# Kernel tuning notes

Hardware: AMD Instinct MI355X
Metric: run time of the kernel (lower is better)

## Reference

```python
import jax, jax.numpy as jnp
import numpy as np

EPS = 1e-5

def _bn(x, gamma, beta, axes):
    # batch-norm with batch statistics (torch training-mode forward, biased var)
    mu = jnp.mean(x, axis=axes, keepdims=True)
    var = jnp.var(x, axis=axes, keepdims=True)
    shape = [1] * x.ndim
    shape[1] = -1  # channel dim is axis 1
    return (x - mu) * jax.lax.rsqrt(var + EPS) * gamma.reshape(shape) + beta.reshape(shape)

def setup_inputs() -> dict:
    key = jax.random.key(0)
    k1, k2, k3, k4, k5 = jax.random.split(key, 5)
    N, H, D, L, M, C = 8, 8, 64, 1024, 1024, 64
    scale = 1.0 / np.sqrt(D)
    return {
        "query": jax.random.normal(k1, (N, H, D, L), dtype=jnp.float32) * scale,
        "key": jax.random.normal(k2, (N, H, D, M), dtype=jnp.float32) * scale,
        "value": jax.random.normal(k3, (N, H, C, M), dtype=jnp.float32),
        "gamma_sim": jnp.ones((H,), dtype=jnp.float32),
        "beta_sim": jnp.zeros((H,), dtype=jnp.float32),
        "gamma_v": jnp.ones((H * C,), dtype=jnp.float32),
        "beta_v": jnp.zeros((H * C,), dtype=jnp.float32),
    }

def reference(query, key, value, gamma_sim, beta_sim, gamma_v, beta_v):
    N, H, D, L = query.shape
    C = value.shape[2]
    # QK^T -> [N, H, L, M]
    logits = jnp.einsum('bhdl,bhdm->bhlm', query, key)
    # BatchNorm2d over channel=head: stats over (N, L, M)
    logits = _bn(logits, gamma_sim, beta_sim, axes=(0, 2, 3))
    # softmax in fp32 (autocast(enabled=False) + .float())
    weights = jax.nn.softmax(logits.astype(jnp.float32), axis=-1)
    # AV -> [N, H, D_v, L] then flatten heads
    rv = jnp.einsum('bhlm,bhdm->bhdl', weights, value).reshape(N, H * C, L)
    # BatchNorm1d over channel: stats over (N, L)
    rv = _bn(rv, gamma_v, beta_v, axes=(0, 2))
    # torch F.gelu default is exact (erf-based)
    return jax.nn.gelu(rv, approximate=False)
```

## Files before the change

kernel.cpp:

```cpp
#include <hip/hip_runtime.h>
#include <hip/hip_bf16.h>
#include <math.h>


typedef __attribute__((ext_vector_type(4)))  float    f32x4;
typedef __attribute__((ext_vector_type(16))) float    f32x16;
typedef __attribute__((ext_vector_type(8)))  __bf16   bf16x8;
typedef __attribute__((ext_vector_type(8)))  short    s16x8;
typedef __attribute__((ext_vector_type(4)))  short    s16x4;
typedef __attribute__((ext_vector_type(2)))  unsigned u32x2;
typedef __attribute__((ext_vector_type(4)))  unsigned u32x4;

#define KT_OFF 0u
#define VB_OFF (8u*1024u*1024u)
#define P1_OFF (16u*1024u*1024u)
#define RS_OFF (24u*1024u*1024u)
#define GM_OFF (32u*1024u*1024u)
#define SPLIT_WS_NEED (24u*1024u*1024u + 512u*1024u + 4096u)
#define GRAM2_WS_NEED (48u*1024u*1024u)

static __device__ __forceinline__ short bf16s(float f) {
  return __builtin_bit_cast(short, (__bf16)f);
}
static __device__ __forceinline__ unsigned pkbf(float lo, float hi) {
  unsigned l = (unsigned)__builtin_bit_cast(unsigned short, (__bf16)lo);
  unsigned h = (unsigned)__builtin_bit_cast(unsigned short, (__bf16)hi);
  return l | (h << 16);
}
static __device__ __forceinline__ float bf2f(short s) {
  return __builtin_bit_cast(float, ((unsigned)(unsigned short)s) << 16);
}
static __device__ __forceinline__ bf16x8 cvt8(const float* p) {
  f32x4 a = *(const f32x4*)p;
  f32x4 b = *(const f32x4*)(p + 4);
  bf16x8 r;
  r[0]=(__bf16)a[0]; r[1]=(__bf16)a[1]; r[2]=(__bf16)a[2]; r[3]=(__bf16)a[3];
  r[4]=(__bf16)b[0]; r[5]=(__bf16)b[1]; r[6]=(__bf16)b[2]; r[7]=(__bf16)b[3];
  return r;
}
static __device__ __forceinline__ f32x16 z16() {
  f32x16 z;
  #pragma unroll
  for (int i = 0; i < 16; ++i) z[i] = 0.f;
  return z;
}
static __device__ __forceinline__ bf16x8 mk8(unsigned a, unsigned b, unsigned c, unsigned d) {
  u32x4 u; u[0]=a; u[1]=b; u[2]=c; u[3]=d;
  return __builtin_bit_cast(bf16x8, u);
}
static __device__ __forceinline__ void gll16(const void* g, void* l) {
  __builtin_amdgcn_global_load_lds(
      (const __attribute__((address_space(1))) void*)g,
      (__attribute__((address_space(3))) void*)l, 16, 0, 0);
}

__global__ __launch_bounds__(256) void k0_prep(const float* __restrict__ K,
                                               const float* __restrict__ V,
                                               short* __restrict__ Kt,
                                               short* __restrict__ Vb) {
  int tid = threadIdx.x;
  if (blockIdx.x < 1024) {
    int bh = blockIdx.x >> 4;
    int m0 = (blockIdx.x & 15) << 6;
    __shared__ short tile[64][72];
    int d = tid >> 2;
    #pragma unroll
    for (int it = 0; it < 4; ++it) {
      int mc4 = (tid & 3) + (it << 2);
      const f32x4 v = *(const f32x4*)(K + (((size_t)(bh*64 + d)) << 10) + m0 + (mc4 << 2));
      #pragma unroll
      for (int j = 0; j < 4; ++j) tile[mc4*4 + j][d] = bf16s(v[j]);
    }
    __syncthreads();
    int m = tid >> 2, q = tid & 3;
    s16x8 o0, o1;
    #pragma unroll
    for (int j = 0; j < 8; ++j) { o0[j] = tile[m][q*16 + j]; o1[j] = tile[m][q*16 + 8 + j]; }
    short* dst = Kt + ((size_t)bh << 16) + ((size_t)(m0 + m) << 6) + (q << 4);
    *(s16x8*)dst = o0;
    *(s16x8*)(dst + 8) = o1;
  } else {
    size_t base = ((size_t)(blockIdx.x - 1024)) << 13;
    #pragma unroll
    for (int it = 0; it < 8; ++it) {
      size_t idx = base + ((size_t)it << 10) + (tid << 2);
      f32x4 x = *(const f32x4*)(V + idx);
      s16x4 y;
      #pragma unroll
      for (int j = 0; j < 4; ++j) y[j] = bf16s(x[j]);
      *(s16x4*)(Vb + idx) = y;
    }
  }
}

__global__ __launch_bounds__(256) void k1a_gram(const float* __restrict__ Q,
                                                const float* __restrict__ K,
                                                float* __restrict__ gm) {
  int bh = blockIdx.x >> 3, sl = blockIdx.x & 7;
  int tid = threadIdx.x, w = tid >> 6, lane = tid & 63;
  int l31 = lane & 31, hi = lane >> 5;
  const float* qlo = Q + ((size_t)bh << 16) + ((size_t)l31 << 10);
  const float* qhi = qlo + (32u << 10);
  const float* klo = K + ((size_t)bh << 16) + ((size_t)l31 << 10);
  const float* khi = klo + (32u << 10);
  f32x16 gq00 = z16(), gq01 = z16(), gq11 = z16();
  f32x16 gk00 = z16(), gk01 = z16(), gk11 = z16();
  #pragma unroll
  for (int lc = 0; lc < 2; ++lc) {
    int loff = (sl << 7) + (w << 5) + (lc << 4) + (hi << 3);
    bf16x8 aql = cvt8(qlo + loff), aqh = cvt8(qhi + loff);
    bf16x8 akl = cvt8(klo + loff), akh = cvt8(khi + loff);
    gq00 = __builtin_amdgcn_mfma_f32_32x32x16_bf16(aql, aql, gq00, 0, 0, 0);
    gq01 = __builtin_amdgcn_mfma_f32_32x32x16_bf16(aql, aqh, gq01, 0, 0, 0);
    gq11 = __builtin_amdgcn_mfma_f32_32x32x16_bf16(aqh, aqh, gq11, 0, 0, 0);
    gk00 = __builtin_amdgcn_mfma_f32_32x32x16_bf16(akl, akl, gk00, 0, 0, 0);
    gk01 = __builtin_amdgcn_mfma_f32_32x32x16_bf16(akl, akh, gk01, 0, 0, 0);
    gk11 = __builtin_amdgcn_mfma_f32_32x32x16_bf16(akh, akh, gk11, 0, 0, 0);
  }
  __shared__ float RQ[4][64][16];
  __shared__ float RK[4][64][16];
  float* gout = gm + ((size_t)blockIdx.x * 6144u);
  #define K1A_RED(GQ_, GK_, TI_)                                            \
    __syncthreads();                                                        \
    _Pragma("unroll")                                                       \
    for (int r = 0; r < 16; ++r) { RQ[w][lane][r] = GQ_[r]; RK[w][lane][r] = GK_[r]; } \
    __syncthreads();                                                        \
    {                                                                       \
      int e = tid & 63, rq = (tid >> 6) << 2;                               \
      f32x4 aq, ak;                                                         \
      _Pragma("unroll")                                                     \
      for (int j = 0; j < 4; ++j) {                                         \
        int r = rq + j;                                                     \
        aq[j] = RQ[0][e][r] + RQ[1][e][r] + RQ[2][e][r] + RQ[3][e][r];      \
        ak[j] = RK[0][e][r] + RK[1][e][r] + RK[2][e][r] + RK[3][e][r];      \
      }                                                                     \
      *(f32x4*)(gout + (TI_)*1024 + (e << 4) + rq) = aq;                    \
      *(f32x4*)(gout + ((TI_) + 3)*1024 + (e << 4) + rq) = ak;              \
    }
  K1A_RED(gq00, gk00, 0)
  K1A_RED(gq01, gk01, 1)
  K1A_RED(gq11, gk11, 2)
  #undef K1A_RED
}

__global__ __launch_bounds__(256) void k1b_dot(const float* __restrict__ gm,
                                               float* __restrict__ ss) {
  int bh = blockIdx.x;
  int tid = threadIdx.x, w = tid >> 6, lane = tid & 63;
  float part = 0.f;
  #pragma unroll
  for (int t = 0; t < 3; ++t) {
    f32x4 aq = {0.f, 0.f, 0.f, 0.f}, ak = {0.f, 0.f, 0.f, 0.f};
    #pragma unroll
    for (int s = 0; s < 8; ++s) {
      const float* base = gm + ((size_t)((bh << 3) + s) * 6144u) + (size_t)t*1024u + (tid << 2);
      aq += *(const f32x4*)base;
      ak += *(const f32x4*)(base + 3*1024);
    }
    float d = aq[0]*ak[0] + aq[1]*ak[1] + aq[2]*ak[2] + aq[3]*ak[3];
    part += (t == 1) ? 2.0f * d : d;
  }
  #pragma unroll
  for (int off = 32; off > 0; off >>= 1) part += __shfl_down(part, off, 64);
  __shared__ float red[4];
  if (lane == 0) red[w] = part;
  __syncthreads();
  if (tid == 0) ss[bh] = red[0] + red[1] + red[2] + red[3];
}

__global__ __launch_bounds__(512) void k1_gram(const float* __restrict__ Q,
                                               const float* __restrict__ K,
                                               float* __restrict__ ss) {
  int bh = blockIdx.x;
  int tid = threadIdx.x, w = tid >> 6, lane = tid & 63;
  int l31 = lane & 31, hi = lane >> 5;
  const float* qlo = Q + ((size_t)bh << 16) + ((size_t)l31 << 10);
  const float* qhi = qlo + (32u << 10);
  const float* klo = K + ((size_t)bh << 16) + ((size_t)l31 << 10);
  const float* khi = klo + (32u << 10);
  f32x16 gq00 = z16(), gq01 = z16(), gq11 = z16();
  f32x16 gk00 = z16(), gk01 = z16(), gk11 = z16();
  for (int lc = 0; lc < 8; ++lc) {
    int loff = (w << 7) + (lc << 4) + (hi << 3);
    bf16x8 aql = cvt8(qlo + loff), aqh = cvt8(qhi + loff);
    bf16x8 akl = cvt8(klo + loff), akh = cvt8(khi + loff);
    gq00 = __builtin_amdgcn_mfma_f32_32x32x16_bf16(aql, aql, gq00, 0, 0, 0);
    gq01 = __builtin_amdgcn_mfma_f32_32x32x16_bf16(aql, aqh, gq01, 0, 0, 0);
    gq11 = __builtin_amdgcn_mfma_f32_32x32x16_bf16(aqh, aqh, gq11, 0, 0, 0);
    gk00 = __builtin_amdgcn_mfma_f32_32x32x16_bf16(akl, akl, gk00, 0, 0, 0);
    gk01 = __builtin_amdgcn_mfma_f32_32x32x16_bf16(akl, akh, gk01, 0, 0, 0);
    gk11 = __builtin_amdgcn_mfma_f32_32x32x16_bf16(akh, akh, gk11, 0, 0, 0);
  }
  __shared__ float RQ[8][64][16];
  __shared__ float RK[8][64][16];
  float part = 0.f;
  #define K1_REDUCE(GQ_, GK_, WT_)                                          \
    __syncthreads();                                                        \
    _Pragma("unroll")                                                       \
    for (int r = 0; r < 16; ++r) { RQ[w][lane][r] = GQ_[r]; RK[w][lane][r] = GK_[r]; } \
    __syncthreads();                                                        \
    if (tid < 256) {                                                        \
      int e = tid & 63, rq = (tid >> 6) << 2;                               \
      _Pragma("unroll")                                                     \
      for (int j = 0; j < 4; ++j) {                                         \
        int r = rq + j;                                                     \
        float aq = 0.f, ak = 0.f;                                           \
        _Pragma("unroll")                                                   \
        for (int ww = 0; ww < 8; ++ww) { aq += RQ[ww][e][r]; ak += RK[ww][e][r]; } \
        part += (WT_) * aq * ak;                                            \
      }                                                                     \
    }
  K1_REDUCE(gq00, gk00, 1.0f)
  K1_REDUCE(gq01, gk01, 2.0f)
  K1_REDUCE(gq11, gk11, 1.0f)
  #undef K1_REDUCE
  #pragma unroll
  for (int off = 32; off > 0; off >>= 1) part += __shfl_down(part, off, 64);
  __shared__ float red[8];
  __syncthreads();
  if (lane == 0) red[w] = part;
  __syncthreads();
  if (tid == 0) {
    float s = 0.f;
    #pragma unroll
    for (int ww = 0; ww < 8; ++ww) s += red[ww];
    ss[bh] = s;
  }
}

template<bool SPLIT>
__global__ __launch_bounds__(256) void k2_attn(const float* __restrict__ Q,
                                               const short* __restrict__ Kt,
                                               const short* __restrict__ Vbf,
                                               const float* __restrict__ ss,
                                               const float* __restrict__ gsim,
                                               float* __restrict__ rv,
                                               short* __restrict__ p1,
                                               float* __restrict__ rsp) {
  __shared__ short ldsK[2][4096];
  __shared__ short ldsV[2][4096];
  int b = blockIdx.x;
  int bh   = (b & 7) + (((b >> 3) & 7) << 3);
  int rest = b >> 6;
  int slab  = SPLIT ? (rest >> 1) : rest;
  int mh    = SPLIT ? (rest & 1) : 0;
  int tbase = mh << 3;
  const int TT = SPLIT ? 8 : 16;
  int l0 = slab << 7;
  int tid = threadIdx.x, w = tid >> 6, lane = tid & 63;
  int l31 = lane & 31, hi = lane >> 5;
  int lq = l0 + (w << 5) + l31;

  int h = bh & 7;
  float ssum = 0.f;
  #pragma unroll
  for (int nb = 0; nb < 8; ++nb) ssum += ss[(nb << 3) + h];
  float scf = gsim[h] * rsqrtf(ssum * (1.0f / 8388608.0f) + 1e-5f) * 1.44269504089f;

  const short* ktb = Kt  + ((size_t)bh << 16);
  const short* vbb = Vbf + ((size_t)bh << 16);
  const float* qb  = Q   + ((size_t)bh << 16) + lq;

  bf16x8 qf[4];
  #pragma unroll
  for (int kc = 0; kc < 4; ++kc) {
    bf16x8 f;
    #pragma unroll
    for (int i = 0; i < 8; ++i)
      f[i] = (__bf16)(qb[(size_t)((kc << 4) + (hi << 3) + i) << 10] * scf);
    qf[kc] = f;
  }

  int koff[2][4], voff[2][2][2];
  #pragma unroll
  for (int mt = 0; mt < 2; ++mt) {
    int mrow = (mt << 5) + l31;
    #pragma unroll
    for (int kc = 0; kc < 4; ++kc) {
      int chunk = (kc << 1) + hi;
      koff[mt][kc] = mrow*128 + ((chunk << 4) ^ ((mrow & 7) << 4));
    }
    #pragma unroll
    for (int cz = 0; cz < 2; ++cz) {
      int crow = (cz << 5) + l31;
      #pragma unroll
      for (int j = 0; j < 2; ++j) {
        int chunk = (mt << 2) + (j << 1) + hi;
        voff[mt][cz][j] = crow*128 + ((chunk << 4) ^ ((crow & 7) << 4));
      }
    }
  }

  {
    int m0 = tbase << 6;
    #pragma unroll
    for (int p = 0; p < 2; ++p) {
      int idx = (p << 8) + tid, row = idx >> 3, ch = idx & 7;
      gll16(ktb + ((size_t)(m0 + row) << 6) + ((ch ^ (row & 7)) << 3), &ldsK[0][idx << 3]);
      gll16(vbb + ((size_t)row << 10) + m0 + ((ch ^ (row & 7)) << 3), &ldsV[0][idx << 3]);
    }
  }
  __syncthreads();

  f32x16 o0 = z16(), o1 = z16();
  float rsum = 0.f;

  for (int t = 0; t < TT; ++t) {
    int cur = t & 1, nxt = cur ^ 1;
    if (t < TT - 1) {
      int m1 = (tbase + t + 1) << 6;
      #pragma unroll
      for (int p = 0; p < 2; ++p) {
        int idx = (p << 8) + tid, row = idx >> 3, ch = idx & 7;
        gll16(ktb + ((size_t)(m1 + row) << 6) + ((ch ^ (row & 7)) << 3), &ldsK[nxt][idx << 3]);
        gll16(vbb + ((size_t)row << 10) + m1 + ((ch ^ (row & 7)) << 3), &ldsV[nxt][idx << 3]);
      }
    }
    #pragma unroll
    for (int mt = 0; mt < 2; ++mt) {
      f32x16 s = z16();
      __builtin_amdgcn_s_setprio(1);
      #pragma unroll
      for (int kc = 0; kc < 4; ++kc) {
        bf16x8 af = *(bf16x8*)((char*)&ldsK[cur][0] + koff[mt][kc]);
        s = __builtin_amdgcn_mfma_f32_32x32x16_bf16(af, qf[kc], s, 0, 0, 0);
      }
      __builtin_amdgcn_s_setprio(0);
      float p[16];
      #pragma unroll
      for (int r = 0; r < 16; ++r) { p[r] = __builtin_amdgcn_exp2f(s[r]); rsum += p[r]; }
      unsigned dw[8];
      #pragma unroll
      for (int j = 0; j < 8; ++j) dw[j] = pkbf(p[2*j], p[2*j+1]);
      u32x2 a0 = __builtin_amdgcn_permlane32_swap(dw[0], dw[2], false, false);
      u32x2 a1 = __builtin_amdgcn_permlane32_swap(dw[1], dw[3], false, false);
      u32x2 a2 = __builtin_amdgcn_permlane32_swap(dw[4], dw[6], false, false);
      u32x2 a3 = __builtin_amdgcn_permlane32_swap(dw[5], dw[7], false, false);
      bf16x8 pb0 = mk8(a0[0], a1[0], a0[1], a1[1]);
      bf16x8 pb1 = mk8(a2[0], a3[0], a2[1], a3[1]);
      __builtin_amdgcn_s_setprio(1);
      {
        bf16x8 va0 = *(bf16x8*)((char*)&ldsV[cur][0] + voff[mt][0][0]);
        o0 = __builtin_amdgcn_mfma_f32_32x32x16_bf16(va0, pb0, o0, 0, 0, 0);
        bf16x8 va1 = *(bf16x8*)((char*)&ldsV[cur][0] + voff[mt][0][1]);
        o0 = __builtin_amdgcn_mfma_f32_32x32x16_bf16(va1, pb1, o0, 0, 0, 0);
      }
      {
        bf16x8 va0 = *(bf16x8*)((char*)&ldsV[cur][0] + voff[mt][1][0]);
        o1 = __builtin_amdgcn_mfma_f32_32x32x16_bf16(va0, pb0, o1, 0, 0, 0);
        bf16x8 va1 = *(bf16x8*)((char*)&ldsV[cur][0] + voff[mt][1][1]);
        o1 = __builtin_amdgcn_mfma_f32_32x32x16_bf16(va1, pb1, o1, 0, 0, 0);
      }
      __builtin_amdgcn_s_setprio(0);
    }
    __syncthreads();
  }

  float tot = rsum + __shfl_xor(rsum, 32, 64);
  if constexpr (!SPLIT) {
    float inv = 1.0f / tot;
    #pragma unroll
    for (int r = 0; r < 16; ++r) {
      int cr = (r & 3) + ((r >> 2) << 3) + (hi << 2);
      rv[((size_t)(bh*64 + cr) << 10) + lq] = o0[r] * inv;
    }
    #pragma unroll
    for (int r = 0; r < 16; ++r) {
      int cr = 32 + (r & 3) + ((r >> 2) << 3) + (hi << 2);
      rv[((size_t)(bh*64 + cr) << 10) + lq] = o1[r] * inv;
    }
  } else {
    if (mh == 0) {
      #pragma unroll
      for (int r = 0; r < 16; ++r) {
        int cr = (r & 3) + ((r >> 2) << 3) + (hi << 2);
        rv[((size_t)(bh*64 + cr) << 10) + lq] = o0[r];
      }
      #pragma unroll
      for (int r = 0; r < 16; ++r) {
        int cr = 32 + (r & 3) + ((r >> 2) << 3) + (hi << 2);
        rv[((size_t)(bh*64 + cr) << 10) + lq] = o1[r];
      }
    } else {
      #pragma unroll
      for (int r = 0; r < 16; ++r) {
        int cr = (r & 3) + ((r >> 2) << 3) + (hi << 2);
        p1[((size_t)(bh*64 + cr) << 10) + lq] = bf16s(o0[r]);
      }
      #pragma unroll
      for (int r = 0; r < 16; ++r) {
        int cr = 32 + (r & 3) + ((r >> 2) << 3) + (hi << 2);
        p1[((size_t)(bh*64 + cr) << 10) + lq] = bf16s(o1[r]);
      }
    }
    if (hi == 0) rsp[(mh << 16) + (bh << 10) + lq] = tot;
  }
}

template<bool SPLIT>
__global__ __launch_bounds__(256) void k34_bn_gelu(const float* rv,
                                                   const short* __restrict__ p1,
                                                   const float* __restrict__ rsp,
                                                   const float* __restrict__ gamma_v,
                                                   const float* __restrict__ beta_v,
                                                   float* out) {
  int ch = blockIdx.x;
  int h  = ch >> 6;
  int tid = threadIdx.x, w = tid >> 6, lane = tid & 63;
  f32x4 xr[8];
  float s = 0.f, s2 = 0.f;
  #pragma unroll
  for (int b = 0; b < 8; ++b) {
    size_t roff = (((size_t)(b*512 + ch)) << 10) + (tid << 2);
    f32x4 x = *(const f32x4*)(rv + roff);
    if constexpr (SPLIT) {
      s16x4 pp = *(const s16x4*)(p1 + roff);
      size_t soff = (((size_t)(b*8 + h)) << 10) + (tid << 2);
      f32x4 r0 = *(const f32x4*)(rsp + soff);
      f32x4 r1 = *(const f32x4*)(rsp + 65536 + soff);
      #pragma unroll
      for (int j = 0; j < 4; ++j)
        x[j] = (x[j] + bf2f(pp[j])) / (r0[j] + r1[j]);
    }
    xr[b] = x;
    #pragma unroll
    for (int j = 0; j < 4; ++j) { s += x[j]; s2 += x[j]*x[j]; }
  }
  #pragma unroll
  for (int off = 32; off > 0; off >>= 1) { s += __shfl_down(s, off, 64); s2 += __shfl_down(s2, off, 64); }
  __shared__ float red0[4], red1[4];
  __shared__ float ab[2];
  if (lane == 0) { red0[w] = s; red1[w] = s2; }
  __syncthreads();
  if (tid == 0) {
    float S  = red0[0] + red0[1] + red0[2] + red0[3];
    float S2 = red1[0] + red1[1] + red1[2] + red1[3];
    float mean = S * (1.0f / 8192.0f);
    float var  = S2 * (1.0f / 8192.0f) - mean * mean;
    float a = gamma_v[ch] * rsqrtf(var + 1e-5f);
    ab[0] = a; ab[1] = beta_v[ch] - mean * a;
  }
  __syncthreads();
  float a = ab[0], bb = ab[1];
  #pragma unroll
  for (int b = 0; b < 8; ++b) {
    size_t off = (((size_t)(b*512 + ch)) << 10) + (tid << 2);
    f32x4 y;
    #pragma unroll
    for (int j = 0; j < 4; ++j) {
      float v = a * xr[b][j] + bb;
      y[j] = 0.5f * v * (1.0f + erff(v * 0.70710678118f));
    }
    *(f32x4*)(out + off) = y;
  }
}

extern "C" void kernel_launch(void* const* d_in, const int* in_sizes, int n_in,
                              void* d_out, int out_size, void* d_ws, size_t ws_size,
                              hipStream_t stream) {
  const float* q        = (const float*)d_in[0];
  const float* k        = (const float*)d_in[1];
  const float* v        = (const float*)d_in[2];
  const float* gamma_s  = (const float*)d_in[3];
  const float* gamma_v  = (const float*)d_in[5];
  const float* beta_v   = (const float*)d_in[6];
  float* out = (float*)d_out;
  char*  ws  = (char*)d_ws;
  short* kt  = (short*)(ws + KT_OFF);
  short* vbf = (short*)(ws + VB_OFF);
  short* p1  = (short*)(ws + P1_OFF);
  float* rsp = (float*)(ws + RS_OFF);
  float* gm  = (float*)(ws + GM_OFF);

  const bool split_ok = ws_size >= (size_t)SPLIT_WS_NEED;
  const bool gram2_ok = ws_size >= (size_t)GRAM2_WS_NEED;
  size_t tail = split_ok ? (size_t)(24u*1024u*1024u + 512u*1024u)
                         : (size_t)(16u*1024u*1024u);
  float* ss = (float*)(ws + tail);

  k0_prep<<<1536, 256, 0, stream>>>(k, v, kt, vbf);
  if (gram2_ok) {
    k1a_gram<<<512, 256, 0, stream>>>(q, k, gm);
    k1b_dot <<<64, 256, 0, stream>>>(gm, ss);
  } else {
    k1_gram<<<64, 512, 0, stream>>>(q, k, ss);
  }
  if (split_ok) {
    k2_attn<true ><<<1024, 256, 0, stream>>>(q, kt, vbf, ss, gamma_s, out, p1, rsp);
    k34_bn_gelu<true ><<<512, 256, 0, stream>>>(out, p1, rsp, gamma_v, beta_v, out);
  } else {
    k2_attn<false><<<512, 256, 0, stream>>>(q, kt, vbf, ss, gamma_s, out, p1, rsp);
    k34_bn_gelu<false><<<512, 256, 0, stream>>>(out, p1, rsp, gamma_v, beta_v, out);
  }
}
```

Before: 73.17 us.

## Fuse K/V prep with Gram partials and double attention tile per barrier

The K/V bf16 conversion kernel and the Gram-partial kernel are merged into one 2048-block launch that shares an LDS arena, removing a launch and letting both phases run concurrently. The attention kernel now stages two 64-column tiles per pipeline step, which halves the number of __syncthreads in the main loop and drops the final barrier. It also removes the s_setprio hints. The cost is doubled LDS for K/V buffers (32KB), which may reduce occupancy, plus a larger combined prep kernel.

```diff
diff --git a/kernel.cpp b/kernel.cpp
--- a/kernel.cpp
+++ b/kernel.cpp
@@ -52,6 +52,123 @@
   __builtin_amdgcn_global_load_lds(
       (const __attribute__((address_space(1))) void*)g,
       (__attribute__((address_space(3))) void*)l, 16, 0, 0);
+}
+
+__global__ __launch_bounds__(256) void k01_prep(const float* __restrict__ K,
+                                                const float* __restrict__ V,
+                                                const float* __restrict__ Q,
+                                                short* __restrict__ Kt,
+                                                short* __restrict__ Vb,
+                                                float* __restrict__ gm) {
+  __shared__ float arena_f[8192];
+  int tid = threadIdx.x;
+  int bid = blockIdx.x;
+  if (bid < 1024) {
+    short* tile = (short*)arena_f;
+    int bh = bid >> 4;
+    int m0 = (bid & 15) << 6;
+    int d = tid >> 2;
+    #pragma unroll
+    for (int it = 0; it < 4; ++it) {
+      int mc4 = (tid & 3) + (it << 2);
+      const f32x4 v = *(const f32x4*)(K + (((size_t)(bh*64 + d)) << 10) + m0 + (mc4 << 2));
+      #pragma unroll
+      for (int j = 0; j < 4; ++j) tile[(mc4*4 + j)*72 + d] = bf16s(v[j]);
+    }
+    __syncthreads();
+    int m = tid >> 2, q = tid & 3;
+    s16x8 o0, o1;
+    #pragma unroll
+    for (int j = 0; j < 8; ++j) { o0[j] = tile[m*72 + q*16 + j]; o1[j] = tile[m*72 + q*16 + 8 + j]; }
+    short* dst = Kt + ((size_t)bh << 16) + ((size_t)(m0 + m) << 6) + (q << 4);
+    *(s16x8*)dst = o0;
+    *(s16x8*)(dst + 8) = o1;
+  } else if (bid < 1536) {
+    size_t base = ((size_t)(bid - 1024)) << 13;
+    #pragma unroll
+    for (int it = 0; it < 8; ++it) {
+      size_t idx = base + ((size_t)it << 10) + (tid << 2);
+      f32x4 x = *(const f32x4*)(V + idx);
+      s16x4 y;
+      #pragma unroll
+      for (int j = 0; j < 4; ++j) y[j] = bf16s(x[j]);
+      *(s16x4*)(Vb + idx) = y;
+    }
+  } else {
+    int b2 = bid - 1536;
+    int bh = b2 >> 3, sl = b2 & 7;
+    int w = tid >> 6, lane = tid & 63;
+    int l31 = lane & 31, hi = lane >> 5;
+    const float* qlo = Q + ((size_t)bh << 16) + ((size_t)l31 << 10);
+    const float* qhi = qlo + (32u << 10);
+    const float* klo = K + ((size_t)bh << 16) + ((size_t)l31 << 10);
+    const float* khi = klo + (32u << 10);
+    f32x16 gq00 = z16(), gq01 = z16(), gq11 = z16();
+    f32x16 gk00 = z16(), gk01 = z16(), gk11 = z16();
+    #pragma unroll
+    for (int lc = 0; lc < 2; ++lc) {
+      int loff = (sl << 7) + (w << 5) + (lc << 4) + (hi << 3);
+      bf16x8 aql = cvt8(qlo + loff), aqh = cvt8(qhi + loff);
+      bf16x8 akl = cvt8(klo + loff), akh = cvt8(khi + loff);
+      gq00 = __builtin_amdgcn_mfma_f32_32x32x16_bf16(aql, aql, gq00, 0, 0, 0);
+      gq01 = __builtin_amdgcn_mfma_f32_32x32x16_bf16(aql, aqh, gq01, 0, 0, 0);
+      gq11 = __builtin_amdgcn_mfma_f32_32x32x16_bf16(aqh, aqh, gq11, 0, 0, 0);
+      gk00 = __builtin_amdgcn_mfma_f32_32x32x16_bf16(akl, akl, gk00, 0, 0, 0);
+      gk01 = __builtin_amdgcn_mfma_f32_32x32x16_bf16(akl, akh, gk01, 0, 0, 0);
+      gk11 = __builtin_amdgcn_mfma_f32_32x32x16_bf16(akh, akh, gk11, 0, 0, 0);
+    }
+    float* RQ = arena_f;
+    float* RK = arena_f + 4096;
+    float* gout = gm + ((size_t)b2 * 6144u);
+    #define K1A_RED(GQ_, GK_, TI_)                                            \
+      __syncthreads();                                                        \
+      _Pragma("unroll")                                                       \
+      for (int r = 0; r < 16; ++r) {                                          \
+        RQ[w*1024 + lane*16 + r] = GQ_[r]; RK[w*1024 + lane*16 + r] = GK_[r]; \
+      }                                                                       \
+      __syncthreads();                                                        \
+      {                                                                       \
+        int e = tid & 63, rq = (tid >> 6) << 2;                               \
+        f32x4 aq, ak;                                                         \
+        _Pragma("unroll")                                                     \
+        for (int j = 0; j < 4; ++j) {                                         \
+          int r = rq + j;                                                     \
+          aq[j] = RQ[e*16+r] + RQ[1024+e*16+r] + RQ[2048+e*16+r] + RQ[3072+e*16+r]; \
+          ak[j] = RK[e*16+r] + RK[1024+e*16+r] + RK[2048+e*16+r] + RK[3072+e*16+r]; \
+        }                                                                     \
+        *(f32x4*)(gout + (TI_)*1024 + (e << 4) + rq) = aq;                    \
+        *(f32x4*)(gout + ((TI_) + 3)*1024 + (e << 4) + rq) = ak;              \
+      }
+    K1A_RED(gq00, gk00, 0)
+    K1A_RED(gq01, gk01, 1)
+    K1A_RED(gq11, gk11, 2)
+    #undef K1A_RED
+  }
+}
+
+__global__ __launch_bounds__(256) void k1b_dot(const float* __restrict__ gm,
+                                               float* __restrict__ ss) {
+  int bh = blockIdx.x;
+  int tid = threadIdx.x, w = tid >> 6, lane = tid & 63;
+  float part = 0.f;
+  #pragma unroll
+  for (int t = 0; t < 3; ++t) {
+    f32x4 aq = {0.f, 0.f, 0.f, 0.f}, ak = {0.f, 0.f, 0.f, 0.f};
+    #pragma unroll
+    for (int s = 0; s < 8; ++s) {
+      const float* base = gm + ((size_t)((bh << 3) + s) * 6144u) + (size_t)t*1024u + (tid << 2);
+      aq += *(const f32x4*)base;
+      ak += *(const f32x4*)(base + 3*1024);
+    }
+    float d = aq[0]*ak[0] + aq[1]*ak[1] + aq[2]*ak[2] + aq[3]*ak[3];
+    part += (t == 1) ? 2.0f * d : d;
+  }
+  #pragma unroll
+  for (int off = 32; off > 0; off >>= 1) part += __shfl_down(part, off, 64);
+  __shared__ float red[4];
+  if (lane == 0) red[w] = part;
+  __syncthreads();
+  if (tid == 0) ss[bh] = red[0] + red[1] + red[2] + red[3];
 }
 
 __global__ __launch_bounds__(256) void k0_prep(const float* __restrict__ K,
@@ -91,81 +208,6 @@
       *(s16x4*)(Vb + idx) = y;
     }
   }
-}
-
-__global__ __launch_bounds__(256) void k1a_gram(const float* __restrict__ Q,
-                                                const float* __restrict__ K,
-                                                float* __restrict__ gm) {
-  int bh = blockIdx.x >> 3, sl = blockIdx.x & 7;
-  int tid = threadIdx.x, w = tid >> 6, lane = tid & 63;
-  int l31 = lane & 31, hi = lane >> 5;
-  const float* qlo = Q + ((size_t)bh << 16) + ((size_t)l31 << 10);
-  const float* qhi = qlo + (32u << 10);
-  const float* klo = K + ((size_t)bh << 16) + ((size_t)l31 << 10);
-  const float* khi = klo + (32u << 10);
-  f32x16 gq00 = z16(), gq01 = z16(), gq11 = z16();
-  f32x16 gk00 = z16(), gk01 = z16(), gk11 = z16();
-  #pragma unroll
-  for (int lc = 0; lc < 2; ++lc) {
-    int loff = (sl << 7) + (w << 5) + (lc << 4) + (hi << 3);
-    bf16x8 aql = cvt8(qlo + loff), aqh = cvt8(qhi + loff);
-    bf16x8 akl = cvt8(klo + loff), akh = cvt8(khi + loff);
-    gq00 = __builtin_amdgcn_mfma_f32_32x32x16_bf16(aql, aql, gq00, 0, 0, 0);
-    gq01 = __builtin_amdgcn_mfma_f32_32x32x16_bf16(aql, aqh, gq01, 0, 0, 0);
-    gq11 = __builtin_amdgcn_mfma_f32_32x32x16_bf16(aqh, aqh, gq11, 0, 0, 0);
-    gk00 = __builtin_amdgcn_mfma_f32_32x32x16_bf16(akl, akl, gk00, 0, 0, 0);
-    gk01 = __builtin_amdgcn_mfma_f32_32x32x16_bf16(akl, akh, gk01, 0, 0, 0);
-    gk11 = __builtin_amdgcn_mfma_f32_32x32x16_bf16(akh, akh, gk11, 0, 0, 0);
-  }
-  __shared__ float RQ[4][64][16];
-  __shared__ float RK[4][64][16];
-  float* gout = gm + ((size_t)blockIdx.x * 6144u);
-  #define K1A_RED(GQ_, GK_, TI_)                                            \
-    __syncthreads();                                                        \
-    _Pragma("unroll")                                                       \
-    for (int r = 0; r < 16; ++r) { RQ[w][lane][r] = GQ_[r]; RK[w][lane][r] = GK_[r]; } \
-    __syncthreads();                                                        \
-    {                                                                       \
-      int e = tid & 63, rq = (tid >> 6) << 2;                               \
-      f32x4 aq, ak;                                                         \
-      _Pragma("unroll")                                                     \
-      for (int j = 0; j < 4; ++j) {                                         \
-        int r = rq + j;                                                     \
-        aq[j] = RQ[0][e][r] + RQ[1][e][r] + RQ[2][e][r] + RQ[3][e][r];      \
-        ak[j] = RK[0][e][r] + RK[1][e][r] + RK[2][e][r] + RK[3][e][r];      \
-      }                                                                     \
-      *(f32x4*)(gout + (TI_)*1024 + (e << 4) + rq) = aq;                    \
-      *(f32x4*)(gout + ((TI_) + 3)*1024 + (e << 4) + rq) = ak;              \
-    }
-  K1A_RED(gq00, gk00, 0)
-  K1A_RED(gq01, gk01, 1)
-  K1A_RED(gq11, gk11, 2)
-  #undef K1A_RED
-}
-
-__global__ __launch_bounds__(256) void k1b_dot(const float* __restrict__ gm,
-                                               float* __restrict__ ss) {
-  int bh = blockIdx.x;
-  int tid = threadIdx.x, w = tid >> 6, lane = tid & 63;
-  float part = 0.f;
-  #pragma unroll
-  for (int t = 0; t < 3; ++t) {
-    f32x4 aq = {0.f, 0.f, 0.f, 0.f}, ak = {0.f, 0.f, 0.f, 0.f};
-    #pragma unroll
-    for (int s = 0; s < 8; ++s) {
-      const float* base = gm + ((size_t)((bh << 3) + s) * 6144u) + (size_t)t*1024u + (tid << 2);
-      aq += *(const f32x4*)base;
-      ak += *(const f32x4*)(base + 3*1024);
-    }
-    float d = aq[0]*ak[0] + aq[1]*ak[1] + aq[2]*ak[2] + aq[3]*ak[3];
-    part += (t == 1) ? 2.0f * d : d;
-  }
-  #pragma unroll
-  for (int off = 32; off > 0; off >>= 1) part += __shfl_down(part, off, 64);
-  __shared__ float red[4];
-  if (lane == 0) red[w] = part;
-  __syncthreads();
-  if (tid == 0) ss[bh] = red[0] + red[1] + red[2] + red[3];
 }
 
 __global__ __launch_bounds__(512) void k1_gram(const float* __restrict__ Q,
@@ -237,15 +279,15 @@
                                                float* __restrict__ rv,
                                                short* __restrict__ p1,
                                                float* __restrict__ rsp) {
-  __shared__ short ldsK[2][4096];
-  __shared__ short ldsV[2][4096];
+  __shared__ short ldsK[2][2][4096];
+  __shared__ short ldsV[2][2][4096];
   int b = blockIdx.x;
   int bh   = (b & 7) + (((b >> 3) & 7) << 3);
   int rest = b >> 6;
   int slab  = SPLIT ? (rest >> 1) : rest;
   int mh    = SPLIT ? (rest & 1) : 0;
   int tbase = mh << 3;
-  const int TT = SPLIT ? 8 : 16;
+  const int NP = SPLIT ? 4 : 8;
   int l0 = slab << 7;
   int tid = threadIdx.x, w = tid >> 6, lane = tid & 63;
   int l31 = lane & 31, hi = lane >> 5;
@@ -291,70 +333,67 @@
     }
   }
 
-  {
-    int m0 = tbase << 6;
-    #pragma unroll
-    for (int p = 0; p < 2; ++p) {
-      int idx = (p << 8) + tid, row = idx >> 3, ch = idx & 7;
-      gll16(ktb + ((size_t)(m0 + row) << 6) + ((ch ^ (row & 7)) << 3), &ldsK[0][idx << 3]);
-      gll16(vbb + ((size_t)row << 10) + m0 + ((ch ^ (row & 7)) << 3), &ldsV[0][idx << 3]);
-    }
-  }
-  __syncthreads();
-
   f32x16 o0 = z16(), o1 = z16();
   float rsum = 0.f;
 
-  for (int t = 0; t < TT; ++t) {
-    int cur = t & 1, nxt = cur ^ 1;
-    if (t < TT - 1) {
-      int m1 = (tbase + t + 1) << 6;
-      #pragma unroll
-      for (int p = 0; p < 2; ++p) {
-        int idx = (p << 8) + tid, row = idx >> 3, ch = idx & 7;
-        gll16(ktb + ((size_t)(m1 + row) << 6) + ((ch ^ (row & 7)) << 3), &ldsK[nxt][idx << 3]);
-        gll16(vbb + ((size_t)row << 10) + m1 + ((ch ^ (row & 7)) << 3), &ldsV[nxt][idx << 3]);
-      }
-    }
-    #pragma unroll
-    for (int mt = 0; mt < 2; ++mt) {
-      f32x16 s = z16();
-      __builtin_amdgcn_s_setprio(1);
-      #pragma unroll
-      for (int kc = 0; kc < 4; ++kc) {
-        bf16x8 af = *(bf16x8*)((char*)&ldsK[cur][0] + koff[mt][kc]);
-        s = __builtin_amdgcn_mfma_f32_32x32x16_bf16(af, qf[kc], s, 0, 0, 0);
-      }
-      __builtin_amdgcn_s_setprio(0);
-      float p[16];
-      #pragma unroll
-      for (int r = 0; r < 16; ++r) { p[r] = __builtin_amdgcn_exp2f(s[r]); rsum += p[r]; }
-      unsigned dw[8];
-      #pragma unroll
-      for (int j = 0; j < 8; ++j) dw[j] = pkbf(p[2*j], p[2*j+1]);
-      u32x2 a0 = __builtin_amdgcn_permlane32_swap(dw[0], dw[2], false, false);
-      u32x2 a1 = __builtin_amdgcn_permlane32_swap(dw[1], dw[3], false, false);
-      u32x2 a2 = __builtin_amdgcn_permlane32_swap(dw[4], dw[6], false, false);
-      u32x2 a3 = __builtin_amdgcn_permlane32_swap(dw[5], dw[7], false, false);
-      bf16x8 pb0 = mk8(a0[0], a1[0], a0[1], a1[1]);
-      bf16x8 pb1 = mk8(a2[0], a3[0], a2[1], a3[1]);
-      __builtin_amdgcn_s_setprio(1);
-      {
-        bf16x8 va0 = *(bf16x8*)((char*)&ldsV[cur][0] + voff[mt][0][0]);
-        o0 = __builtin_amdgcn_mfma_f32_32x32x16_bf16(va0, pb0, o0, 0, 0, 0);
-        bf16x8 va1 = *(bf16x8*)((char*)&ldsV[cur][0] + voff[mt][0][1]);
-        o0 = __builtin_amdgcn_mfma_f32_32x32x16_bf16(va1, pb1, o0, 0, 0, 0);
-      }
-      {
-        bf16x8 va0 = *(bf16x8*)((char*)&ldsV[cur][0] + voff[mt][1][0]);
-        o1 = __builtin_amdgcn_mfma_f32_32x32x16_bf16(va0, pb0, o1, 0, 0, 0);
-        bf16x8 va1 = *(bf16x8*)((char*)&ldsV[cur][0] + voff[mt][1][1]);
-        o1 = __builtin_amdgcn_mfma_f32_32x32x16_bf16(va1, pb1, o1, 0, 0, 0);
-      }
-      __builtin_amdgcn_s_setprio(0);
-    }
-    __syncthreads();
-  }
+  #define STAGE(TT_, PB_, SB_) {                                              \
+    int m0s = (tbase + (TT_)) << 6;                                           \
+    _Pragma("unroll")                                                         \
+    for (int p = 0; p < 2; ++p) {                                             \
+      int idx = (p << 8) + tid, row = idx >> 3, ch = idx & 7;                 \
+      gll16(ktb + ((size_t)(m0s + row) << 6) + ((ch ^ (row & 7)) << 3), &ldsK[PB_][SB_][idx << 3]); \
+      gll16(vbb + ((size_t)row << 10) + m0s + ((ch ^ (row & 7)) << 3), &ldsV[PB_][SB_][idx << 3]);  \
+    } }
+
+  #define COMPUTE(PB_, SB_)                                                   \
+    _Pragma("unroll")                                                         \
+    for (int mt = 0; mt < 2; ++mt) {                                          \
+      f32x16 s = z16();                                                       \
+      _Pragma("unroll")                                                       \
+      for (int kc = 0; kc < 4; ++kc) {                                        \
+        bf16x8 af = *(bf16x8*)((char*)&ldsK[PB_][SB_][0] + koff[mt][kc]);     \
+        s = __builtin_amdgcn_mfma_f32_32x32x16_bf16(af, qf[kc], s, 0, 0, 0);  \
+      }                                                                       \
+      float p[16];                                                            \
+      _Pragma("unroll")                                                       \
+      for (int r = 0; r < 16; ++r) { p[r] = __builtin_amdgcn_exp2f(s[r]); rsum += p[r]; } \
+      unsigned dw[8];                                                         \
+      _Pragma("unroll")                                                       \
+      for (int j = 0; j < 8; ++j) dw[j] = pkbf(p[2*j], p[2*j+1]);             \
+      u32x2 a0 = __builtin_amdgcn_permlane32_swap(dw[0], dw[2], false, false); \
+      u32x2 a1 = __builtin_amdgcn_permlane32_swap(dw[1], dw[3], false, false); \
+      u32x2 a2 = __builtin_amdgcn_permlane32_swap(dw[4], dw[6], false, false); \
+      u32x2 a3 = __builtin_amdgcn_permlane32_swap(dw[5], dw[7], false, false); \
+      bf16x8 pb0 = mk8(a0[0], a1[0], a0[1], a1[1]);                           \
+      bf16x8 pb1 = mk8(a2[0], a3[0], a2[1], a3[1]);                           \
+      {                                                                       \
+        bf16x8 va0 = *(bf16x8*)((char*)&ldsV[PB_][SB_][0] + voff[mt][0][0]);  \
+        o0 = __builtin_amdgcn_mfma_f32_32x32x16_bf16(va0, pb0, o0, 0, 0, 0);  \
+        bf16x8 va1 = *(bf16x8*)((char*)&ldsV[PB_][SB_][0] + voff[mt][0][1]);  \
+        o0 = __builtin_amdgcn_mfma_f32_32x32x16_bf16(va1, pb1, o0, 0, 0, 0);  \
+      }                                                                       \
+      {                                                                       \
+        bf16x8 va0 = *(bf16x8*)((char*)&ldsV[PB_][SB_][0] + voff[mt][1][0]);  \
+        o1 = __builtin_amdgcn_mfma_f32_32x32x16_bf16(va0, pb0, o1, 0, 0, 0);  \
+        bf16x8 va1 = *(bf16x8*)((char*)&ldsV[PB_][SB_][0] + voff[mt][1][1]);  \
+        o1 = __builtin_amdgcn_mfma_f32_32x32x16_bf16(va1, pb1, o1, 0, 0, 0);  \
+      }                                                                       \
+    }
+
+  STAGE(0, 0, 0) STAGE(1, 0, 1)
+  __syncthreads();
+  for (int pr = 0; pr < NP; ++pr) {
+    int cur = pr & 1, nxt = cur ^ 1;
+    if (pr < NP - 1) {
+      STAGE(2*pr + 2, nxt, 0)
+      STAGE(2*pr + 3, nxt, 1)
+    }
+    COMPUTE(cur, 0)
+    COMPUTE(cur, 1)
+    if (pr < NP - 1) __syncthreads();
+  }
+  #undef STAGE
+  #undef COMPUTE
 
   float tot = rsum + __shfl_xor(rsum, 32, 64);
   if constexpr (!SPLIT) {
@@ -478,11 +517,11 @@
                          : (size_t)(16u*1024u*1024u);
   float* ss = (float*)(ws + tail);
 
-  k0_prep<<<1536, 256, 0, stream>>>(k, v, kt, vbf);
   if (gram2_ok) {
-    k1a_gram<<<512, 256, 0, stream>>>(q, k, gm);
+    k01_prep<<<2048, 256, 0, stream>>>(k, v, q, kt, vbf, gm);
     k1b_dot <<<64, 256, 0, stream>>>(gm, ss);
   } else {
+    k0_prep<<<1536, 256, 0, stream>>>(k, v, kt, vbf);
     k1_gram<<<64, 512, 0, stream>>>(q, k, ss);
   }
   if (split_ok) {
```

Result: slower. 81.98 us (+12.0%).

## Replace split-M attention with 8-wave blocks over 256 query rows

Applied to the files above, without the earlier changes.

Drops the split-M attention path, which wrote bf16 partials and row sums that the BN kernel then merged. Now a single kernel runs 512-thread blocks where each wave handles 32 query rows, for 256 rows per block, and walks all of M. Each K/V tile staged in LDS is shared by twice as many waves, and the partial-sum traffic and merge arithmetic go away. In exchange the grid shrinks to 256 blocks, which may underfill the GPU's CUs and lengthen the serial M loop.

```diff
diff --git a/kernel.cpp b/kernel.cpp
--- a/kernel.cpp
+++ b/kernel.cpp
@@ -13,10 +13,9 @@
 
 #define KT_OFF 0u
 #define VB_OFF (8u*1024u*1024u)
-#define P1_OFF (16u*1024u*1024u)
-#define RS_OFF (24u*1024u*1024u)
+#define SS_OFF (16u*1024u*1024u)
 #define GM_OFF (32u*1024u*1024u)
-#define SPLIT_WS_NEED (24u*1024u*1024u + 512u*1024u + 4096u)
+#define BASE_WS_NEED (16u*1024u*1024u + 4096u)
 #define GRAM2_WS_NEED (48u*1024u*1024u)
 
 static __device__ __forceinline__ short bf16s(float f) {
@@ -26,9 +25,6 @@
   unsigned l = (unsigned)__builtin_bit_cast(unsigned short, (__bf16)lo);
   unsigned h = (unsigned)__builtin_bit_cast(unsigned short, (__bf16)hi);
   return l | (h << 16);
-}
-static __device__ __forceinline__ float bf2f(short s) {
-  return __builtin_bit_cast(float, ((unsigned)(unsigned short)s) << 16);
 }
 static __device__ __forceinline__ bf16x8 cvt8(const float* p) {
   f32x4 a = *(const f32x4*)p;
@@ -228,25 +224,18 @@
   }
 }
 
-template<bool SPLIT>
-__global__ __launch_bounds__(256) void k2_attn(const float* __restrict__ Q,
-                                               const short* __restrict__ Kt,
-                                               const short* __restrict__ Vbf,
-                                               const float* __restrict__ ss,
-                                               const float* __restrict__ gsim,
-                                               float* __restrict__ rv,
-                                               short* __restrict__ p1,
-                                               float* __restrict__ rsp) {
+__global__ __launch_bounds__(512) void k2_attn8(const float* __restrict__ Q,
+                                                const short* __restrict__ Kt,
+                                                const short* __restrict__ Vbf,
+                                                const float* __restrict__ ss,
+                                                const float* __restrict__ gsim,
+                                                float* __restrict__ rv) {
   __shared__ short ldsK[2][4096];
   __shared__ short ldsV[2][4096];
   int b = blockIdx.x;
   int bh   = (b & 7) + (((b >> 3) & 7) << 3);
-  int rest = b >> 6;
-  int slab  = SPLIT ? (rest >> 1) : rest;
-  int mh    = SPLIT ? (rest & 1) : 0;
-  int tbase = mh << 3;
-  const int TT = SPLIT ? 8 : 16;
-  int l0 = slab << 7;
+  int slab = b >> 6;
+  int l0 = slab << 8;
   int tid = threadIdx.x, w = tid >> 6, lane = tid & 63;
   int l31 = lane & 31, hi = lane >> 5;
   int lq = l0 + (w << 5) + l31;
@@ -292,29 +281,22 @@
   }
 
   {
-    int m0 = tbase << 6;
-    #pragma unroll
-    for (int p = 0; p < 2; ++p) {
-      int idx = (p << 8) + tid, row = idx >> 3, ch = idx & 7;
-      gll16(ktb + ((size_t)(m0 + row) << 6) + ((ch ^ (row & 7)) << 3), &ldsK[0][idx << 3]);
-      gll16(vbb + ((size_t)row << 10) + m0 + ((ch ^ (row & 7)) << 3), &ldsV[0][idx << 3]);
-    }
+    int row = tid >> 3, ch = tid & 7;
+    gll16(ktb + ((size_t)row << 6) + ((ch ^ (row & 7)) << 3), &ldsK[0][tid << 3]);
+    gll16(vbb + ((size_t)row << 10) + ((ch ^ (row & 7)) << 3), &ldsV[0][tid << 3]);
   }
   __syncthreads();
 
   f32x16 o0 = z16(), o1 = z16();
   float rsum = 0.f;
 
-  for (int t = 0; t < TT; ++t) {
+  for (int t = 0; t < 16; ++t) {
     int cur = t & 1, nxt = cur ^ 1;
-    if (t < TT - 1) {
-      int m1 = (tbase + t + 1) << 6;
-      #pragma unroll
-      for (int p = 0; p < 2; ++p) {
-        int idx = (p << 8) + tid, row = idx >> 3, ch = idx & 7;
-        gll16(ktb + ((size_t)(m1 + row) << 6) + ((ch ^ (row & 7)) << 3), &ldsK[nxt][idx << 3]);
-        gll16(vbb + ((size_t)row << 10) + m1 + ((ch ^ (row & 7)) << 3), &ldsV[nxt][idx << 3]);
-      }
+    if (t < 15) {
+      int m1 = (t + 1) << 6;
+      int row = tid >> 3, ch = tid & 7;
+      gll16(ktb + ((size_t)(m1 + row) << 6) + ((ch ^ (row & 7)) << 3), &ldsK[nxt][tid << 3]);
+      gll16(vbb + ((size_t)row << 10) + m1 + ((ch ^ (row & 7)) << 3), &ldsV[nxt][tid << 3]);
     }
     #pragma unroll
     for (int mt = 0; mt < 2; ++mt) {
@@ -357,55 +339,24 @@
   }
 
   float tot = rsum + __shfl_xor(rsum, 32, 64);
-  if constexpr (!SPLIT) {
-    float inv = 1.0f / tot;
-    #pragma unroll
-    for (int r = 0; r < 16; ++r) {
-      int cr = (r & 3) + ((r >> 2) << 3) + (hi << 2);
-      rv[((size_t)(bh*64 + cr) << 10) + lq] = o0[r] * inv;
-    }
-    #pragma unroll
-    for (int r = 0; r < 16; ++r) {
-      int cr = 32 + (r & 3) + ((r >> 2) << 3) + (hi << 2);
-      rv[((size_t)(bh*64 + cr) << 10) + lq] = o1[r] * inv;
-    }
-  } else {
-    if (mh == 0) {
-      #pragma unroll
-      for (int r = 0; r < 16; ++r) {
-        int cr = (r & 3) + ((r >> 2) << 3) + (hi << 2);
-        rv[((size_t)(bh*64 + cr) << 10) + lq] = o0[r];
-      }
-      #pragma unroll
-      for (int r = 0; r < 16; ++r) {
-        int cr = 32 + (r & 3) + ((r >> 2) << 3) + (hi << 2);
-        rv[((size_t)(bh*64 + cr) << 10) + lq] = o1[r];
-      }
-    } else {
-      #pragma unroll
-      for (int r = 0; r < 16; ++r) {
-        int cr = (r & 3) + ((r >> 2) << 3) + (hi << 2);
-        p1[((size_t)(bh*64 + cr) << 10) + lq] = bf16s(o0[r]);
-      }
-      #pragma unroll
-      for (int r = 0; r < 16; ++r) {
-        int cr = 32 + (r & 3) + ((r >> 2) << 3) + (hi << 2);
-        p1[((size_t)(bh*64 + cr) << 10) + lq] = bf16s(o1[r]);
-      }
-    }
-    if (hi == 0) rsp[(mh << 16) + (bh << 10) + lq] = tot;
-  }
-}
-
-template<bool SPLIT>
+  float inv = 1.0f / tot;
+  #pragma unroll
+  for (int r = 0; r < 16; ++r) {
+    int cr = (r & 3) + ((r >> 2) << 3) + (hi << 2);
+    rv[((size_t)(bh*64 + cr) << 10) + lq] = o0[r] * inv;
+  }
+  #pragma unroll
+  for (int r = 0; r < 16; ++r) {
+    int cr = 32 + (r & 3) + ((r >> 2) << 3) + (hi << 2);
+    rv[((size_t)(bh*64 + cr) << 10) + lq] = o1[r] * inv;
+  }
+}
+
 __global__ __launch_bounds__(256) void k34_bn_gelu(const float* rv,
-                                                   const short* __restrict__ p1,
-                                                   const float* __restrict__ rsp,
                                                    const float* __restrict__ gamma_v,
                                                    const float* __restrict__ beta_v,
                                                    float* out) {
   int ch = blockIdx.x;
-  int h  = ch >> 6;
   int tid = threadIdx.x, w = tid >> 6, lane = tid & 63;
   f32x4 xr[8];
   float s = 0.f, s2 = 0.f;
@@ -413,15 +364,6 @@
   for (int b = 0; b < 8; ++b) {
     size_t roff = (((size_t)(b*512 + ch)) << 10) + (tid << 2);
     f32x4 x = *(const f32x4*)(rv + roff);
-    if constexpr (SPLIT) {
-      s16x4 pp = *(const s16x4*)(p1 + roff);
-      size_t soff = (((size_t)(b*8 + h)) << 10) + (tid << 2);
-      f32x4 r0 = *(const f32x4*)(rsp + soff);
-      f32x4 r1 = *(const f32x4*)(rsp + 65536 + soff);
-      #pragma unroll
-      for (int j = 0; j < 4; ++j)
-        x[j] = (x[j] + bf2f(pp[j])) / (r0[j] + r1[j]);
-    }
     xr[b] = x;
     #pragma unroll
     for (int j = 0; j < 4; ++j) { s += x[j]; s2 += x[j]*x[j]; }
@@ -468,15 +410,10 @@
   char*  ws  = (char*)d_ws;
   short* kt  = (short*)(ws + KT_OFF);
   short* vbf = (short*)(ws + VB_OFF);
-  short* p1  = (short*)(ws + P1_OFF);
-  float* rsp = (float*)(ws + RS_OFF);
+  float* ss  = (float*)(ws + SS_OFF);
   float* gm  = (float*)(ws + GM_OFF);
 
-  const bool split_ok = ws_size >= (size_t)SPLIT_WS_NEED;
   const bool gram2_ok = ws_size >= (size_t)GRAM2_WS_NEED;
-  size_t tail = split_ok ? (size_t)(24u*1024u*1024u + 512u*1024u)
-                         : (size_t)(16u*1024u*1024u);
-  float* ss = (float*)(ws + tail);
 
   k0_prep<<<1536, 256, 0, stream>>>(k, v, kt, vbf);
   if (gram2_ok) {
@@ -485,11 +422,6 @@
   } else {
     k1_gram<<<64, 512, 0, stream>>>(q, k, ss);
   }
-  if (split_ok) {
-    k2_attn<true ><<<1024, 256, 0, stream>>>(q, kt, vbf, ss, gamma_s, out, p1, rsp);
-    k34_bn_gelu<true ><<<512, 256, 0, stream>>>(out, p1, rsp, gamma_v, beta_v, out);
-  } else {
-    k2_attn<false><<<512, 256, 0, stream>>>(q, kt, vbf, ss, gamma_s, out, p1, rsp);
-    k34_bn_gelu<false><<<512, 256, 0, stream>>>(out, p1, rsp, gamma_v, beta_v, out);
-  }
-}
+  k2_attn8<<<256, 512, 0, stream>>>(q, kt, vbf, ss, gamma_s, out);
+  k34_bn_gelu<<<512, 256, 0, stream>>>(out, gamma_v, beta_v, out);
+}
```

New measurement: 70.68 us. 1.04x faster.
